# Performance work log

Hardware: AMD Instinct MI355X
Metric: run time of the kernel (lower is better)

Reference implementation:

```python
import jax, jax.numpy as jnp
import numpy as np

B, S, D, H, HD = 4, 2048, 1024, 16, 64
MLP = 4 * D
ROPE_BASE = 10000.0
TARGET_SPARSITY = 0.2


def _rotate_half(t):
    return jnp.concatenate([-t[..., HD // 2:], t[..., :HD // 2]], axis=-1)


def setup_inputs() -> dict:
    key = jax.random.key(0)
    ks = jax.random.split(key, 10)
    s = 0.02
    return {
        "x": jax.random.normal(ks[0], (B, S, D), jnp.float32),
        "gate_w": jax.random.normal(ks[1], (D, 1), jnp.float32) * s,
        "gate_b": jnp.zeros((1,), jnp.float32),
        "wq": jax.random.normal(ks[2], (D, D), jnp.float32) * s,
        "wk": jax.random.normal(ks[3], (D, D), jnp.float32) * s,
        "wv": jax.random.normal(ks[4], (D, D), jnp.float32) * s,
        "wo": jax.random.normal(ks[5], (D, D), jnp.float32) * s,
        "conv_w": jax.random.normal(ks[6], (D, 3), jnp.float32) * s,  # depthwise k=3
        "conv_b": jnp.zeros((D,), jnp.float32),
        "mlp_w1": jax.random.normal(ks[7], (D, MLP), jnp.float32) * s,
        "mlp_b1": jnp.zeros((MLP,), jnp.float32),
        "mlp_w2": jax.random.normal(ks[8], (MLP, D), jnp.float32) * s,
        "mlp_b2": jnp.zeros((D,), jnp.float32),
    }


def reference(x, gate_w, gate_b, wq, wk, wv, wo, conv_w, conv_b,
              mlp_w1, mlp_b1, mlp_w2, mlp_b2):
    # --- Router (eval path: hard threshold, mask_ste == active mask) ---
    logits = x @ gate_w + gate_b                    # [B,S,1]
    probs = jax.nn.sigmoid(logits)
    aux_loss = (probs.mean() - TARGET_SPARSITY) ** 2
    mask = (probs > 0.5).astype(x.dtype)            # [B,S,1]

    # --- Reflexive stream: causal depthwise conv (left pad 2) + MLP ---
    xp = jnp.pad(x, ((0, 0), (2, 0), (0, 0)))       # [B,S+2,D]
    x_conv = (xp[:, 0:S] * conv_w[:, 0]
              + xp[:, 1:S + 1] * conv_w[:, 1]
              + xp[:, 2:S + 2] * conv_w[:, 2] + conv_b)
    shallow = jax.nn.relu(x_conv @ mlp_w1 + mlp_b1) @ mlp_w2 + mlp_b2

    # --- Contextual stream: RoPE causal attention, queries gated by router ---
    q = (x @ wq).reshape(B, S, H, HD)
    k = (x @ wk).reshape(B, S, H, HD)
    v = (x @ wv).reshape(B, S, H, HD)

    pos = jnp.arange(S)
    inv_freq = 1.0 / (ROPE_BASE ** (jnp.arange(0, HD, 2, dtype=jnp.float32) / HD))
    freqs = pos[:, None].astype(jnp.float32) * inv_freq[None, :]
    emb = jnp.concatenate([freqs, freqs], axis=-1)  # [S,HD]
    cos = jnp.cos(emb)[None, :, None, :]
    sin = jnp.sin(emb)[None, :, None, :]
    q = q * cos + _rotate_half(q) * sin
    k = k * cos + _rotate_half(k) * sin

    scale = 1.0 / np.sqrt(HD)
    scores = jnp.einsum('bqhd,bkhd->bhqk', q, k) * scale
    causal = pos[:, None] >= pos[None, :]           # [S,S]
    scores = jnp.where(causal[None, None], scores, jnp.finfo(scores.dtype).min)
    attn = jax.nn.softmax(scores, axis=-1)
    ctx = jnp.einsum('bhqk,bkhd->bqhd', attn, v).reshape(B, S, D)
    ctx = (ctx @ wo) * mask                         # scatter back: only active queries contribute

    out = x + shallow + ctx
    return out, aux_loss
```

## Files before the change

kernel.cpp:

```cpp
#include <hip/hip_runtime.h>
#include <hip/hip_bf16.h>

#define DDIM 1024
#define SLEN 2048
#define NTOK 8192
#define MLPD 4096

typedef float f32x4 __attribute__((ext_vector_type(4)));
typedef __bf16 bf16x8 __attribute__((ext_vector_type(8)));

__device__ __forceinline__ void async16(void* lds, const void* g) {
  __builtin_amdgcn_global_load_lds(
      (__attribute__((address_space(1))) void*)g,
      (__attribute__((address_space(3))) void*)lds, 16, 0, 0);
}

__global__ __launch_bounds__(256) void prep_kernel(
    const float* __restrict__ x, const float* __restrict__ gate_w,
    const float* __restrict__ gate_b, const float* __restrict__ conv_w,
    const float* __restrict__ conv_b, __bf16* __restrict__ xb,
    __bf16* __restrict__ xcb, float* __restrict__ maskp,
    float* __restrict__ probsp) {
  const int tok = blockIdx.x, t = threadIdx.x;
  const int s = tok & (SLEN - 1);
  const float* xr = x + (size_t)tok * DDIM;
  float4 v = ((const float4*)xr)[t];
  float4 g = ((const float4*)gate_w)[t];
  float part = v.x * g.x + v.y * g.y + v.z * g.z + v.w * g.w;
#pragma unroll
  for (int d = 32; d; d >>= 1) part += __shfl_down(part, d);
  __shared__ float ws4[4];
  const int lane = t & 63, w = t >> 6;
  if (lane == 0) ws4[w] = part;
  __syncthreads();
  if (t == 0) {
    float logit = ws4[0] + ws4[1] + ws4[2] + ws4[3] + gate_b[0];
    float prob = 1.f / (1.f + __expf(-logit));
    probsp[tok] = prob;
    maskp[tok] = prob > 0.5f ? 1.f : 0.f;
  }
  union { ushort4 u; __bf16 b[4]; } xo;
  xo.b[0] = (__bf16)v.x; xo.b[1] = (__bf16)v.y;
  xo.b[2] = (__bf16)v.z; xo.b[3] = (__bf16)v.w;
  ((ushort4*)(xb + (size_t)tok * DDIM))[t] = xo.u;
  float4 zero4 = {0.f, 0.f, 0.f, 0.f};
  float4 m1 = (s >= 1) ? ((const float4*)(xr - DDIM))[t] : zero4;
  float4 m2 = (s >= 2) ? ((const float4*)(xr - 2 * DDIM))[t] : zero4;
  int d0 = t * 4;
  float vv[4] = {v.x, v.y, v.z, v.w};
  float a1[4] = {m1.x, m1.y, m1.z, m1.w};
  float a2[4] = {m2.x, m2.y, m2.z, m2.w};
  union { ushort4 u; __bf16 b[4]; } co;
#pragma unroll
  for (int i = 0; i < 4; ++i) {
    float c0 = conv_w[(d0 + i) * 3 + 0];
    float c1 = conv_w[(d0 + i) * 3 + 1];
    float c2 = conv_w[(d0 + i) * 3 + 2];
    float r = a2[i] * c0 + a1[i] * c1 + vv[i] * c2 + conv_b[d0 + i];
    co.b[i] = (__bf16)r;
  }
  ((ushort4*)(xcb + (size_t)tok * DDIM))[t] = co.u;
}

__global__ __launch_bounds__(256) void tcast_kernel(const float* __restrict__ src,
                                                    __bf16* __restrict__ dst,
                                                    int K, int N) {
  __shared__ __bf16 tile[64][65];
  const int n0 = blockIdx.x * 64, k0 = blockIdx.y * 64;
  const int t = threadIdx.x;
  const int cr = (t & 15) * 4;
#pragma unroll
  for (int i = 0; i < 4; ++i) {
    int rr = (t >> 4) + i * 16;
    float4 v = *(const float4*)(src + (size_t)(k0 + rr) * N + n0 + cr);
    tile[rr][cr + 0] = (__bf16)v.x; tile[rr][cr + 1] = (__bf16)v.y;
    tile[rr][cr + 2] = (__bf16)v.z; tile[rr][cr + 3] = (__bf16)v.w;
  }
  __syncthreads();
#pragma unroll
  for (int i = 0; i < 2; ++i) {
    int c = t + i * 256;
    int nl = c >> 3, koff = (c & 7) * 8;
    union { uint4 u; __bf16 b[8]; } o;
#pragma unroll
    for (int j = 0; j < 8; ++j) o.b[j] = tile[koff + j][nl];
    *(uint4*)(dst + (size_t)(n0 + nl) * K + k0 + koff) = o.u;
  }
}

template <int EPI>
__global__ __launch_bounds__(256, 2) void gemm_bt(
    const __bf16* __restrict__ A, const __bf16* __restrict__ Bt,
    const float* __restrict__ bias, const float* __restrict__ xres,
    const float* __restrict__ maskp, __bf16* __restrict__ Cb,
    float* __restrict__ Cf, int M, int N, int K) {
  __shared__ char smem[32768];
  char* As = smem;
  char* Bs = smem + 16384;
  const int t = threadIdx.x, lane = t & 63, w = t >> 6;
  const int m0 = blockIdx.y * 128, n0 = blockIdx.x * 128;
  const int wm = (w >> 1) * 64, wn = (w & 1) * 64;
  f32x4 acc[4][4] = {};
  const int nk = K >> 6;
  for (int kt = 0; kt < nk; ++kt) {
    const int k0 = kt << 6;
#pragma unroll
    for (int rd = 0; rd < 4; ++rd) {
      int o = ((rd * 4 + w) << 10) + (lane << 4);
      int row = o >> 7;
      int us = ((o >> 4) & 7) ^ (row & 7);
      async16(As + o, A + (size_t)(m0 + row) * K + k0 + us * 8);
      async16(Bs + o, Bt + (size_t)(n0 + row) * K + k0 + us * 8);
    }
    __syncthreads();
#pragma unroll
    for (int ks = 0; ks < 2; ++ks) {
      bf16x8 af[4], bfr[4];
#pragma unroll
      for (int mt = 0; mt < 4; ++mt) {
        int row = wm + mt * 16 + (lane & 15);
        int u = (ks * 4 + (lane >> 4)) ^ (row & 7);
        af[mt] = *(const bf16x8*)(As + row * 128 + u * 16);
      }
#pragma unroll
      for (int nt = 0; nt < 4; ++nt) {
        int row = wn + nt * 16 + (lane & 15);
        int u = (ks * 4 + (lane >> 4)) ^ (row & 7);
        bfr[nt] = *(const bf16x8*)(Bs + row * 128 + u * 16);
      }
#pragma unroll
      for (int mt = 0; mt < 4; ++mt)
#pragma unroll
        for (int nt = 0; nt < 4; ++nt)
          acc[mt][nt] = __builtin_amdgcn_mfma_f32_16x16x32_bf16(
              af[mt], bfr[nt], acc[mt][nt], 0, 0, 0);
    }
    __syncthreads();
  }
#pragma unroll
  for (int mt = 0; mt < 4; ++mt)
#pragma unroll
    for (int nt = 0; nt < 4; ++nt)
#pragma unroll
      for (int r = 0; r < 4; ++r) {
        int row = m0 + wm + mt * 16 + ((lane >> 4) << 2) + r;
        int col = n0 + wn + nt * 16 + (lane & 15);
        float v = acc[mt][nt][r];
        size_t idx = (size_t)row * N + col;
        if constexpr (EPI == 0) {
          Cb[idx] = (__bf16)v;
        } else if constexpr (EPI == 1) {
          v += bias[col];
          Cb[idx] = (__bf16)fmaxf(v, 0.f);
        } else if constexpr (EPI == 2) {
          Cf[idx] = xres[idx] + v + bias[col];
        } else {
          Cf[idx] += maskp[row] * v;
        }
      }
}

__global__ __launch_bounds__(256) void rope_kernel(__bf16* __restrict__ qkv) {
  const int tok = blockIdx.x, t = threadIdx.x;
  const int s = tok & (SLEN - 1);
#pragma unroll
  for (int pp = 0; pp < 2; ++pp) {
    int p = t + pp * 256;
    int h = p >> 5, i = p & 31;
    float invf = __powf(10000.f, -(float)i * (1.f / 32.f));
    float fr = (float)s * invf;
    float sn = sinf(fr), cs = cosf(fr);
    __bf16* qp = qkv + (size_t)tok * 3072 + h * 64 + i;
    float xq = (float)qp[0], yq = (float)qp[32];
    qp[0] = (__bf16)(xq * cs - yq * sn);
    qp[32] = (__bf16)(yq * cs + xq * sn);
    __bf16* kp = qp + 1024;
    float xk = (float)kp[0], yk = (float)kp[32];
    kp[0] = (__bf16)(xk * cs - yk * sn);
    kp[32] = (__bf16)(yk * cs + xk * sn);
  }
}

__global__ __launch_bounds__(256, 2) void attn_kernel(const __bf16* __restrict__ qkv,
                                                      __bf16* __restrict__ ctx) {
  __shared__ char sm[49152];
  char* Qs = sm;
  char* Ks = sm + 16384;
  char* Vs = sm + 24576;
  char* Ps = sm + 32768;
  const int t = threadIdx.x, lane = t & 63, w = t >> 6;
  const int c = lane & 15, g = lane >> 4, g4 = g * 4;
  const int bh = blockIdx.y, h = bh & 15, b = bh >> 4;
  const size_t tokbase = (size_t)b * SLEN;
  const __bf16* qg = qkv + tokbase * 3072 + h * 64;
  const __bf16* kg = qg + 1024;
  const __bf16* vg = qg + 2048;
  const float SCL = 0.125f * 1.44269504f;

  for (int ph = 0; ph < 2; ++ph) {
    const int qt = ph == 0 ? (int)blockIdx.x : 15 - (int)blockIdx.x;
    const int q0 = qt * 128;
#pragma unroll
    for (int rd = 0; rd < 4; ++rd) {
      int o = ((rd * 4 + w) << 10) + (lane << 4);
      int row = o >> 7;
      int us = ((o >> 4) & 7) ^ (row & 7);
      async16(Qs + o, qg + (size_t)(q0 + row) * 3072 + us * 8);
    }
    __syncthreads();
    bf16x8 qb[2][2];
#pragma unroll
    for (int mt = 0; mt < 2; ++mt)
#pragma unroll
      for (int ks = 0; ks < 2; ++ks) {
        int row = w * 32 + mt * 16 + c;
        int u = (ks * 4 + g) ^ (row & 7);
        qb[mt][ks] = *(const bf16x8*)(Qs + row * 128 + u * 16);
      }

    float m_run[2] = {-1e30f, -1e30f}, l_run[2] = {0.f, 0.f};
    f32x4 o_acc[2][4] = {};
    const int nkt = (q0 + 128) >> 6;
    const int wrow0 = q0 + w * 32;

    for (int kt = 0; kt < nkt; ++kt) {
      const int k0 = kt << 6;
#pragma unroll
      for (int rd = 0; rd < 2; ++rd) {
        int o = ((rd * 4 + w) << 10) + (lane << 4);
        int row = o >> 7;
        int us = ((o >> 4) & 7) ^ (row & 7);
        async16(Ks + o, kg + (size_t)(k0 + row) * 3072 + us * 8);
      }
#pragma unroll
      for (int rnd = 0; rnd < 2; ++rnd) {
        int tok = lane, d0 = w * 8 + rnd * 32;
        union { float4 f; __bf16 bv[8]; } uu;
        uu.f = *(const float4*)(vg + (size_t)(k0 + tok) * 3072 + d0);
#pragma unroll
        for (int j = 0; j < 8; ++j) {
          int d = d0 + j;
          int by = d * 128 + (((tok >> 3) ^ (d & 7)) << 4) + ((tok & 7) << 1);
          *(__bf16*)(Vs + by) = uu.bv[j];
        }
      }
      __syncthreads();
      if (k0 <= wrow0 + 31) {
        f32x4 st[4][2] = {};
#pragma unroll
        for (int ks = 0; ks < 2; ++ks) {
          bf16x8 ka[4];
#pragma unroll
          for (int nt = 0; nt < 4; ++nt) {
            int row = nt * 16 + c;
            int u = (ks * 4 + g) ^ (row & 7);
            ka[nt] = *(const bf16x8*)(Ks + row * 128 + u * 16);
          }
#pragma unroll
          for (int nt = 0; nt < 4; ++nt)
#pragma unroll
            for (int mt = 0; mt < 2; ++mt)
              st[nt][mt] = __builtin_amdgcn_mfma_f32_16x16x32_bf16(
                  ka[nt], qb[mt][ks], st[nt][mt], 0, 0, 0);
        }
        const bool needmask = (k0 + 63) > wrow0;
#pragma unroll
        for (int mt = 0; mt < 2; ++mt) {
          float mx = -1e30f;
          if (needmask) {
            int qglob = wrow0 + mt * 16 + c;
#pragma unroll
            for (int nt = 0; nt < 4; ++nt)
#pragma unroll
              for (int r = 0; r < 4; ++r) {
                float sv = st[nt][mt][r] * SCL;
                if (k0 + nt * 16 + g4 + r > qglob) sv = -1e30f;
                st[nt][mt][r] = sv;
                mx = fmaxf(mx, sv);
              }
          } else {
#pragma unroll
            for (int nt = 0; nt < 4; ++nt)
#pragma unroll
              for (int r = 0; r < 4; ++r) {
                float sv = st[nt][mt][r] * SCL;
                st[nt][mt][r] = sv;
                mx = fmaxf(mx, sv);
              }
          }
          mx = fmaxf(mx, __shfl_xor(mx, 16));
          mx = fmaxf(mx, __shfl_xor(mx, 32));
          float mnew = fmaxf(m_run[mt], mx);
          float fac = __builtin_amdgcn_exp2f(m_run[mt] - mnew);
          m_run[mt] = mnew;
          float rs = 0.f;
#pragma unroll
          for (int nt = 0; nt < 4; ++nt)
#pragma unroll
            for (int r = 0; r < 4; ++r) {
              float p = __builtin_amdgcn_exp2f(st[nt][mt][r] - mnew);
              st[nt][mt][r] = p;
              rs += p;
            }
          rs += __shfl_xor(rs, 16);
          rs += __shfl_xor(rs, 32);
          l_run[mt] = l_run[mt] * fac + rs;
          int rowq = mt * 16 + c;
          int rbase = (w << 12) + rowq * 128 + 8 * (g & 1);
#pragma unroll
          for (int nt = 0; nt < 4; ++nt) {
            int us = (2 * nt + (g >> 1)) ^ (c & 7);
            union { unsigned u; __bf16 bb[2]; } p0, p1;
            p0.bb[0] = (__bf16)st[nt][mt][0]; p0.bb[1] = (__bf16)st[nt][mt][1];
            p1.bb[0] = (__bf16)st[nt][mt][2]; p1.bb[1] = (__bf16)st[nt][mt][3];
            *(unsigned*)(Ps + rbase + us * 16) = p0.u;
            *(unsigned*)(Ps + rbase + us * 16 + 4) = p1.u;
          }
#pragma unroll
          for (int r = 0; r < 4; ++r) {
            float fr = __shfl(fac, g * 20 + r);
#pragma unroll
            for (int dt = 0; dt < 4; ++dt) o_acc[mt][dt][r] *= fr;
          }
        }
#pragma unroll
        for (int ks = 0; ks < 2; ++ks) {
          bf16x8 pa[2], vb[4];
#pragma unroll
          for (int mt = 0; mt < 2; ++mt) {
            int row = mt * 16 + c;
            int u = (ks * 4 + g) ^ (row & 7);
            pa[mt] = *(const bf16x8*)(Ps + (w << 12) + row * 128 + u * 16);
          }
#pragma unroll
          for (int dt = 0; dt < 4; ++dt) {
            int row = dt * 16 + c;
            int u = (ks * 4 + g) ^ (row & 7);
            vb[dt] = *(const bf16x8*)(Vs + row * 128 + u * 16);
          }
#pragma unroll
          for (int mt = 0; mt < 2; ++mt)
#pragma unroll
            for (int dt = 0; dt < 4; ++dt)
              o_acc[mt][dt] = __builtin_amdgcn_mfma_f32_16x16x32_bf16(
                  pa[mt], vb[dt], o_acc[mt][dt], 0, 0, 0);
        }
      }
      __syncthreads();
    }
#pragma unroll
    for (int mt = 0; mt < 2; ++mt)
#pragma unroll
      for (int r = 0; r < 4; ++r) {
        float lr = __shfl(l_run[mt], g * 20 + r);
        float inv = 1.f / lr;
        int tokr = q0 + w * 32 + mt * 16 + g4 + r;
#pragma unroll
        for (int dt = 0; dt < 4; ++dt) {
          int d = dt * 16 + c;
          ctx[(tokbase + tokr) * DDIM + h * 64 + d] =
              (__bf16)(o_acc[mt][dt][r] * inv);
        }
      }
    __syncthreads();
  }
}

__global__ __launch_bounds__(256) void aux_kernel(const float* __restrict__ probsp,
                                                  float* __restrict__ outp) {
  const int t = threadIdx.x;
  float sum = 0.f;
  for (int i = t; i < NTOK; i += 256) sum += probsp[i];
#pragma unroll
  for (int d = 32; d; d >>= 1) sum += __shfl_down(sum, d);
  __shared__ float ws4[4];
  if ((t & 63) == 0) ws4[t >> 6] = sum;
  __syncthreads();
  if (t == 0) {
    float m = (ws4[0] + ws4[1] + ws4[2] + ws4[3]) * (1.f / NTOK) - 0.2f;
    outp[0] = m * m;
  }
}

extern "C" void kernel_launch(void* const* d_in, const int* in_sizes, int n_in,
                              void* d_out, int out_size, void* d_ws, size_t ws_size,
                              hipStream_t stream) {
  const float* x      = (const float*)d_in[0];
  const float* gate_w = (const float*)d_in[1];
  const float* gate_b = (const float*)d_in[2];
  const float* wq     = (const float*)d_in[3];
  const float* wk     = (const float*)d_in[4];
  const float* wv     = (const float*)d_in[5];
  const float* wo     = (const float*)d_in[6];
  const float* conv_w = (const float*)d_in[7];
  const float* conv_b = (const float*)d_in[8];
  const float* mlp_w1 = (const float*)d_in[9];
  const float* mlp_b1 = (const float*)d_in[10];
  const float* mlp_w2 = (const float*)d_in[11];
  const float* mlp_b2 = (const float*)d_in[12];
  float* out = (float*)d_out;

  char* ws = (char*)d_ws;
  const size_t MB = 1ull << 20;
  __bf16* xb     = (__bf16*)(ws + 0);
  __bf16* xcb    = (__bf16*)(ws + 16 * MB);
  __bf16* ctx    = (__bf16*)(ws + 16 * MB);
  __bf16* wqkv_t = (__bf16*)(ws + 32 * MB);
  __bf16* wo_t   = (__bf16*)(ws + 38 * MB);
  __bf16* w1_t   = (__bf16*)(ws + 40 * MB);
  __bf16* w2_t   = (__bf16*)(ws + 48 * MB);
  float*  maskp  = (float*)(ws + 56 * MB);
  float*  probsp = (float*)(ws + 56 * MB + 65536);
  __bf16* h1     = (__bf16*)(ws + 57 * MB);
  __bf16* qkv    = (__bf16*)(ws + 57 * MB);

  prep_kernel<<<NTOK, 256, 0, stream>>>(x, gate_w, gate_b, conv_w, conv_b,
                                        xb, xcb, maskp, probsp);
  tcast_kernel<<<dim3(16, 16), 256, 0, stream>>>(wq, wqkv_t, 1024, 1024);
  tcast_kernel<<<dim3(16, 16), 256, 0, stream>>>(wk, wqkv_t + 1024 * 1024, 1024, 1024);
  tcast_kernel<<<dim3(16, 16), 256, 0, stream>>>(wv, wqkv_t + 2048 * 1024, 1024, 1024);
  tcast_kernel<<<dim3(16, 16), 256, 0, stream>>>(wo, wo_t, 1024, 1024);
  tcast_kernel<<<dim3(64, 16), 256, 0, stream>>>(mlp_w1, w1_t, 1024, 4096);
  tcast_kernel<<<dim3(16, 64), 256, 0, stream>>>(mlp_w2, w2_t, 4096, 1024);

  gemm_bt<1><<<dim3(32, 64), 256, 0, stream>>>(xcb, w1_t, mlp_b1, nullptr, nullptr,
                                               h1, nullptr, NTOK, MLPD, DDIM);
  gemm_bt<2><<<dim3(8, 64), 256, 0, stream>>>(h1, w2_t, mlp_b2, x, nullptr,
                                              nullptr, out, NTOK, DDIM, MLPD);
  gemm_bt<0><<<dim3(24, 64), 256, 0, stream>>>(xb, wqkv_t, nullptr, nullptr, nullptr,
                                               qkv, nullptr, NTOK, 3072, DDIM);
  rope_kernel<<<NTOK, 256, 0, stream>>>(qkv);
  attn_kernel<<<dim3(8, 64), 256, 0, stream>>>(qkv, ctx);
  gemm_bt<3><<<dim3(8, 64), 256, 0, stream>>>(ctx, wo_t, nullptr, nullptr, maskp,
                                              nullptr, out, NTOK, DDIM, DDIM);
  aux_kernel<<<1, 256, 0, stream>>>(probsp, out + (size_t)(out_size - 1));
}
```

Baseline: 412.9 us.

## Double-buffer K/V tiles in attention and add lazy softmax rescaling

The attention kernel now prefetches the next K tile asynchronously and the next V tile into registers during compute, scattering V into a second LDS buffer before the barrier. This removes the load-then-sync stall at the start of each key tile. The per-warp P scratch now reuses the Q region to make room for the double buffers. Online-softmax rescaling of the output accumulator is skipped whenever the row max grows by at most 8 (log2 domain), and P stores are widened to 64-bit. Launch bounds for the GEMM and attention kernels are raised to 3 blocks per CU, which risks register pressure or spills.

```diff
diff --git a/kernel.cpp b/kernel.cpp
--- a/kernel.cpp
+++ b/kernel.cpp
@@ -89,7 +89,7 @@
 }
 
 template <int EPI>
-__global__ __launch_bounds__(256, 2) void gemm_bt(
+__global__ __launch_bounds__(256, 3) void gemm_bt(
     const __bf16* __restrict__ A, const __bf16* __restrict__ Bt,
     const float* __restrict__ bias, const float* __restrict__ xres,
     const float* __restrict__ maskp, __bf16* __restrict__ Cb,
@@ -181,13 +181,24 @@
   }
 }
 
-__global__ __launch_bounds__(256, 2) void attn_kernel(const __bf16* __restrict__ qkv,
+__device__ __forceinline__ void scatterV(char* Vdst, int w, int lane,
+                                         float4 va, float4 vb) {
+  union { float4 f; __bf16 bv[8]; } u0, u1;
+  u0.f = va; u1.f = vb;
+#pragma unroll
+  for (int j = 0; j < 8; ++j) {
+    int d = w * 8 + j;
+    int by = d * 128 + (((lane >> 3) ^ (d & 7)) << 4) + ((lane & 7) << 1);
+    *(__bf16*)(Vdst + by) = u0.bv[j];
+    int d2 = d + 32;
+    int by2 = d2 * 128 + (((lane >> 3) ^ (d2 & 7)) << 4) + ((lane & 7) << 1);
+    *(__bf16*)(Vdst + by2) = u1.bv[j];
+  }
+}
+
+__global__ __launch_bounds__(256, 3) void attn_kernel(const __bf16* __restrict__ qkv,
                                                       __bf16* __restrict__ ctx) {
   __shared__ char sm[49152];
-  char* Qs = sm;
-  char* Ks = sm + 16384;
-  char* Vs = sm + 24576;
-  char* Ps = sm + 32768;
   const int t = threadIdx.x, lane = t & 63, w = t >> 6;
   const int c = lane & 15, g = lane >> 4, g4 = g * 4;
   const int bh = blockIdx.y, h = bh & 15, b = bh >> 4;
@@ -196,16 +207,30 @@
   const __bf16* kg = qg + 1024;
   const __bf16* vg = qg + 2048;
   const float SCL = 0.125f * 1.44269504f;
+  char* Ps = sm + (w << 12);
 
   for (int ph = 0; ph < 2; ++ph) {
     const int qt = ph == 0 ? (int)blockIdx.x : 15 - (int)blockIdx.x;
     const int q0 = qt * 128;
+    int cur = 0;
 #pragma unroll
     for (int rd = 0; rd < 4; ++rd) {
       int o = ((rd * 4 + w) << 10) + (lane << 4);
       int row = o >> 7;
       int us = ((o >> 4) & 7) ^ (row & 7);
-      async16(Qs + o, qg + (size_t)(q0 + row) * 3072 + us * 8);
+      async16(sm + o, qg + (size_t)(q0 + row) * 3072 + us * 8);
+    }
+#pragma unroll
+    for (int rd = 0; rd < 2; ++rd) {
+      int o = ((rd * 4 + w) << 10) + (lane << 4);
+      int row = o >> 7;
+      int us = ((o >> 4) & 7) ^ (row & 7);
+      async16(sm + 16384 + o, kg + (size_t)row * 3072 + us * 8);
+    }
+    {
+      float4 va = *(const float4*)(vg + (size_t)lane * 3072 + w * 8);
+      float4 vb2 = *(const float4*)(vg + (size_t)lane * 3072 + w * 8 + 32);
+      scatterV(sm + 32768, w, lane, va, vb2);
     }
     __syncthreads();
     bf16x8 qb[2][2];
@@ -215,7 +240,7 @@
       for (int ks = 0; ks < 2; ++ks) {
         int row = w * 32 + mt * 16 + c;
         int u = (ks * 4 + g) ^ (row & 7);
-        qb[mt][ks] = *(const bf16x8*)(Qs + row * 128 + u * 16);
+        qb[mt][ks] = *(const bf16x8*)(sm + row * 128 + u * 16);
       }
 
     float m_run[2] = {-1e30f, -1e30f}, l_run[2] = {0.f, 0.f};
@@ -225,26 +250,23 @@
 
     for (int kt = 0; kt < nkt; ++kt) {
       const int k0 = kt << 6;
-#pragma unroll
-      for (int rd = 0; rd < 2; ++rd) {
-        int o = ((rd * 4 + w) << 10) + (lane << 4);
-        int row = o >> 7;
-        int us = ((o >> 4) & 7) ^ (row & 7);
-        async16(Ks + o, kg + (size_t)(k0 + row) * 3072 + us * 8);
-      }
-#pragma unroll
-      for (int rnd = 0; rnd < 2; ++rnd) {
-        int tok = lane, d0 = w * 8 + rnd * 32;
-        union { float4 f; __bf16 bv[8]; } uu;
-        uu.f = *(const float4*)(vg + (size_t)(k0 + tok) * 3072 + d0);
-#pragma unroll
-        for (int j = 0; j < 8; ++j) {
-          int d = d0 + j;
-          int by = d * 128 + (((tok >> 3) ^ (d & 7)) << 4) + ((tok & 7) << 1);
-          *(__bf16*)(Vs + by) = uu.bv[j];
-        }
-      }
-      __syncthreads();
+      char* Kc = sm + 16384 + cur * 8192;
+      char* Vc = sm + 32768 + cur * 8192;
+      const bool pref = (kt + 1) < nkt;
+      float4 va, vb2;
+      if (pref) {
+        const int kn0 = k0 + 64;
+        char* Kn = sm + 16384 + (cur ^ 1) * 8192;
+#pragma unroll
+        for (int rd = 0; rd < 2; ++rd) {
+          int o = ((rd * 4 + w) << 10) + (lane << 4);
+          int row = o >> 7;
+          int us = ((o >> 4) & 7) ^ (row & 7);
+          async16(Kn + o, kg + (size_t)(kn0 + row) * 3072 + us * 8);
+        }
+        va = *(const float4*)(vg + (size_t)(kn0 + lane) * 3072 + w * 8);
+        vb2 = *(const float4*)(vg + (size_t)(kn0 + lane) * 3072 + w * 8 + 32);
+      }
       if (k0 <= wrow0 + 31) {
         f32x4 st[4][2] = {};
 #pragma unroll
@@ -254,7 +276,7 @@
           for (int nt = 0; nt < 4; ++nt) {
             int row = nt * 16 + c;
             int u = (ks * 4 + g) ^ (row & 7);
-            ka[nt] = *(const bf16x8*)(Ks + row * 128 + u * 16);
+            ka[nt] = *(const bf16x8*)(Kc + row * 128 + u * 16);
           }
 #pragma unroll
           for (int nt = 0; nt < 4; ++nt)
@@ -290,9 +312,8 @@
           }
           mx = fmaxf(mx, __shfl_xor(mx, 16));
           mx = fmaxf(mx, __shfl_xor(mx, 32));
-          float mnew = fmaxf(m_run[mt], mx);
-          float fac = __builtin_amdgcn_exp2f(m_run[mt] - mnew);
-          m_run[mt] = mnew;
+          const bool skip = __all(mx - m_run[mt] <= 8.f) != 0;
+          float mnew = skip ? m_run[mt] : fmaxf(m_run[mt], mx);
           float rs = 0.f;
 #pragma unroll
           for (int nt = 0; nt < 4; ++nt)
@@ -304,23 +325,28 @@
             }
           rs += __shfl_xor(rs, 16);
           rs += __shfl_xor(rs, 32);
-          l_run[mt] = l_run[mt] * fac + rs;
+          if (skip) {
+            l_run[mt] += rs;
+          } else {
+            float fac = __builtin_amdgcn_exp2f(m_run[mt] - mnew);
+            m_run[mt] = mnew;
+            l_run[mt] = l_run[mt] * fac + rs;
+#pragma unroll
+            for (int r = 0; r < 4; ++r) {
+              float fr = __shfl(fac, g * 20 + r);
+#pragma unroll
+              for (int dt = 0; dt < 4; ++dt) o_acc[mt][dt][r] *= fr;
+            }
+          }
           int rowq = mt * 16 + c;
-          int rbase = (w << 12) + rowq * 128 + 8 * (g & 1);
+          int rbase = rowq * 128 + 8 * (g & 1);
 #pragma unroll
           for (int nt = 0; nt < 4; ++nt) {
             int us = (2 * nt + (g >> 1)) ^ (c & 7);
-            union { unsigned u; __bf16 bb[2]; } p0, p1;
-            p0.bb[0] = (__bf16)st[nt][mt][0]; p0.bb[1] = (__bf16)st[nt][mt][1];
-            p1.bb[0] = (__bf16)st[nt][mt][2]; p1.bb[1] = (__bf16)st[nt][mt][3];
-            *(unsigned*)(Ps + rbase + us * 16) = p0.u;
-            *(unsigned*)(Ps + rbase + us * 16 + 4) = p1.u;
-          }
-#pragma unroll
-          for (int r = 0; r < 4; ++r) {
-            float fr = __shfl(fac, g * 20 + r);
-#pragma unroll
-            for (int dt = 0; dt < 4; ++dt) o_acc[mt][dt][r] *= fr;
+            union { uint2 v; __bf16 bb[4]; } pp;
+            pp.bb[0] = (__bf16)st[nt][mt][0]; pp.bb[1] = (__bf16)st[nt][mt][1];
+            pp.bb[2] = (__bf16)st[nt][mt][2]; pp.bb[3] = (__bf16)st[nt][mt][3];
+            *(uint2*)(Ps + rbase + us * 16) = pp.v;
           }
         }
 #pragma unroll
@@ -330,13 +356,13 @@
           for (int mt = 0; mt < 2; ++mt) {
             int row = mt * 16 + c;
             int u = (ks * 4 + g) ^ (row & 7);
-            pa[mt] = *(const bf16x8*)(Ps + (w << 12) + row * 128 + u * 16);
+            pa[mt] = *(const bf16x8*)(Ps + row * 128 + u * 16);
           }
 #pragma unroll
           for (int dt = 0; dt < 4; ++dt) {
             int row = dt * 16 + c;
             int u = (ks * 4 + g) ^ (row & 7);
-            vb[dt] = *(const bf16x8*)(Vs + row * 128 + u * 16);
+            vb[dt] = *(const bf16x8*)(Vc + row * 128 + u * 16);
           }
 #pragma unroll
           for (int mt = 0; mt < 2; ++mt)
@@ -346,7 +372,9 @@
                   pa[mt], vb[dt], o_acc[mt][dt], 0, 0, 0);
         }
       }
+      if (pref) scatterV(sm + 32768 + (cur ^ 1) * 8192, w, lane, va, vb2);
       __syncthreads();
+      cur ^= 1;
     }
 #pragma unroll
     for (int mt = 0; mt < 2; ++mt)
```

Measured after the change: 416.4 us. Within noise of the previous version (+0.8%).
